# Optimization experiments

Hardware: AMD Instinct MI355X
Metric: run time of the kernel (lower is better)

The kernel has to match this reference:

```python
import jax, jax.numpy as jnp
import numpy as np

N_HEAD = 12

def _rotate_half(x):
    # interleaved rotation: (-x1, x0, -x3, x2, ...)
    x_even = x[..., ::2]
    x_odd = x[..., 1::2]
    return jnp.stack((-x_odd, x_even), axis=-1).reshape(x.shape)

def _rope_tables(T, D, dtype):
    inv_freq = 1.0 / (10000.0 ** (jnp.arange(0, D, 2, dtype=jnp.float32) / D))
    freqs = jnp.arange(T, dtype=jnp.float32)[:, None] * inv_freq[None, :]  # [T, D/2]
    cos = jnp.repeat(jnp.cos(freqs), 2, axis=-1).astype(dtype)  # [T, D]
    sin = jnp.repeat(jnp.sin(freqs), 2, axis=-1).astype(dtype)
    return cos, sin

def setup_inputs() -> dict:
    key = jax.random.key(0)
    ks = jax.random.split(key, 5)
    B, T, C = 8, 1024, 768
    return {
        "x": jax.random.normal(ks[0], (B, T, C), dtype=jnp.float32),
        "W_attn": jax.random.normal(ks[1], (C, 3 * C), dtype=jnp.float32) * (C ** -0.5),
        "b_attn": jax.random.normal(ks[2], (3 * C,), dtype=jnp.float32) * 0.02,
        "W_proj": jax.random.normal(ks[3], (C, C), dtype=jnp.float32) * (C ** -0.5),
        "b_proj": jax.random.normal(ks[4], (C,), dtype=jnp.float32) * 0.02,
    }

def reference(x, W_attn, b_attn, W_proj, b_proj):
    B, T, C = x.shape
    H = N_HEAD
    D = C // H
    qkv = x @ W_attn + b_attn  # [B, T, 3C]
    q, k, v = jnp.split(qkv, 3, axis=-1)
    # [B, H, T, D]
    q = q.reshape(B, T, H, D).transpose(0, 2, 1, 3)
    k = k.reshape(B, T, H, D).transpose(0, 2, 1, 3)
    v = v.reshape(B, T, H, D).transpose(0, 2, 1, 3)
    cos, sin = _rope_tables(T, D, x.dtype)  # [T, D]
    q = q * cos + _rotate_half(q) * sin
    k = k * cos + _rotate_half(k) * sin
    att = jnp.einsum('bhqd,bhkd->bhqk', q, k) * (D ** -0.5)
    causal = jnp.tril(jnp.ones((T, T), dtype=bool))
    att = jnp.where(causal, att, -jnp.inf)
    att = jax.nn.softmax(att, axis=-1)
    y = jnp.einsum('bhqk,bhkd->bhqd', att, v)  # [B, H, T, D]
    y = y.transpose(0, 2, 1, 3).reshape(B, T, C)
    return y @ W_proj + b_proj
```

## Files before the change

### kernel.cpp

```cpp
#include <hip/hip_runtime.h>
#include <cstdint>
#include <cstddef>

typedef __attribute__((ext_vector_type(8))) short frag8;
typedef __attribute__((ext_vector_type(4))) float facc4;

__device__ __forceinline__ float b2f(unsigned short u) {
  union { unsigned int i; float f; } v; v.i = ((unsigned int)u) << 16; return v.f;
}
__device__ __forceinline__ unsigned short f2b(float f) {
  union { float f; unsigned int i; } v; v.f = f;
  unsigned int u = v.i;
  unsigned int r = (u + 0x7fffu + ((u >> 16) & 1u)) >> 16;
  return (unsigned short)r;
}


__global__ void cvt_f32_bf16_k(const float* __restrict__ in, unsigned short* __restrict__ out, int n8) {
  int i = blockIdx.x * blockDim.x + threadIdx.x;
  if (i >= n8) return;
  const float4* p = (const float4*)in + (size_t)i * 2;
  float4 a = p[0], b = p[1];
  union { unsigned short u[8]; frag8 v; } o;
  o.u[0] = f2b(a.x); o.u[1] = f2b(a.y); o.u[2] = f2b(a.z); o.u[3] = f2b(a.w);
  o.u[4] = f2b(b.x); o.u[5] = f2b(b.y); o.u[6] = f2b(b.z); o.u[7] = f2b(b.w);
  *((frag8*)out + i) = o.v;
}

__global__ void transpose_cvt_k(const float* __restrict__ W, unsigned short* __restrict__ Wt, int R, int Cn) {
  __shared__ float tile[32][33];
  int tx = threadIdx.x, ty = threadIdx.y;
  int c = blockIdx.x * 32 + tx;
  #pragma unroll
  for (int i = 0; i < 32; i += 8)
    tile[ty + i][tx] = W[(size_t)(blockIdx.y * 32 + ty + i) * Cn + c];
  __syncthreads();
  int rr = blockIdx.y * 32 + tx;
  #pragma unroll
  for (int i = 0; i < 32; i += 8)
    Wt[(size_t)(blockIdx.x * 32 + ty + i) * R + rr] = f2b(tile[tx][ty + i]);
}

__global__ void rope_tables_k(float* __restrict__ cosT, float* __restrict__ sinT) {
  int id = blockIdx.x * 256 + threadIdx.x;
  int t = id >> 5, i = id & 31;
  float freq = powf(10000.0f, -(float)i * (1.0f / 32.0f));
  float a = (float)t * freq;
  cosT[id] = cosf(a);
  sinT[id] = sinf(a);
}

__global__ void rope_k(unsigned short* __restrict__ Q, unsigned short* __restrict__ Kb,
                       const float* __restrict__ cosT, const float* __restrict__ sinT) {
  int id = blockIdx.x * 256 + threadIdx.x;
  int i = id & 31;
  int t = (id >> 5) & 1023;
  int bh = id >> 15;
  size_t base = ((size_t)bh << 16) + (size_t)t * 64 + i * 2;
  float c = cosT[(t << 5) + i], s = sinT[(t << 5) + i];
  unsigned int* qp = (unsigned int*)(Q + base);
  unsigned int qu = *qp;
  float q0 = b2f(qu & 0xffffu), q1 = b2f(qu >> 16);
  *qp = (unsigned int)f2b(q0 * c - q1 * s) | ((unsigned int)f2b(q1 * c + q0 * s) << 16);
  unsigned int* kp = (unsigned int*)(Kb + base);
  unsigned int ku = *kp;
  float k0 = b2f(ku & 0xffffu), k1 = b2f(ku >> 16);
  *kp = (unsigned int)f2b(k0 * c - k1 * s) | ((unsigned int)f2b(k1 * c + k0 * s) << 16);
}


#define GLDK 72

template<int EPI>
__global__ __launch_bounds__(256)
void gemm128_k(const unsigned short* __restrict__ A, const unsigned short* __restrict__ Bt,
               const float* __restrict__ bias, float* __restrict__ outF,
               unsigned short* __restrict__ Qo, unsigned short* __restrict__ Ko,
               unsigned short* __restrict__ Vo, int M, int N, int K)
{
  __shared__ unsigned short As[128 * GLDK];
  __shared__ unsigned short Bs[128 * GLDK];
  const int tid = threadIdx.x;
  const int lane = tid & 63;
  const int w = tid >> 6, wm = w >> 1, wn = w & 1;
  const int g = lane >> 4, cL = lane & 15;
  const int tM = blockIdx.y * 128, tN = blockIdx.x * 128;

  facc4 zero4 = {0.f, 0.f, 0.f, 0.f};
  facc4 acc[4][4];
  #pragma unroll
  for (int i = 0; i < 4; ++i)
    #pragma unroll
    for (int j = 0; j < 4; ++j) acc[i][j] = zero4;

  const int sr = tid >> 3;
  const int sc = (tid & 7) * 8;

  for (int k0 = 0; k0 < K; k0 += 64) {
    #pragma unroll
    for (int ch = 0; ch < 4; ++ch) {
      int r = sr + ch * 32;
      frag8 va = *(const frag8*)(A  + (size_t)(tM + r) * K + k0 + sc);
      frag8 vb = *(const frag8*)(Bt + (size_t)(tN + r) * K + k0 + sc);
      *(frag8*)(&As[r * GLDK + sc]) = va;
      *(frag8*)(&Bs[r * GLDK + sc]) = vb;
    }
    __syncthreads();
    #pragma unroll
    for (int kk = 0; kk < 2; ++kk) {
      frag8 af[4], bfr[4];
      #pragma unroll
      for (int i = 0; i < 4; ++i)
        af[i] = *(const frag8*)(&As[(wm * 64 + i * 16 + cL) * GLDK + kk * 32 + g * 8]);
      #pragma unroll
      for (int j = 0; j < 4; ++j)
        bfr[j] = *(const frag8*)(&Bs[(wn * 64 + j * 16 + cL) * GLDK + kk * 32 + g * 8]);
      #pragma unroll
      for (int i = 0; i < 4; ++i)
        #pragma unroll
        for (int j = 0; j < 4; ++j)
          acc[i][j] = __builtin_amdgcn_mfma_f32_16x16x32_bf16(af[i], bfr[j], acc[i][j], 0, 0, 0);
    }
    __syncthreads();
  }

  #pragma unroll
  for (int i = 0; i < 4; ++i) {
    #pragma unroll
    for (int j = 0; j < 4; ++j) {
      const int col = tN + wn * 64 + j * 16 + cL;
      const float bv = bias[col];
      if constexpr (EPI == 0) {
        const int sel = col / 768;
        const int cc = col - sel * 768;
        const int h = cc >> 6, d = cc & 63;
        #pragma unroll
        for (int r = 0; r < 4; ++r) {
          const int m = tM + wm * 64 + i * 16 + g * 4 + r;
          const float v = acc[i][j][r] + bv;
          const int b = m >> 10, t = m & 1023;
          const size_t hb = ((size_t)(b * 12 + h)) << 16;
          if (sel == 0)      Qo[hb + (size_t)t * 64 + d] = f2b(v * 0.125f);
          else if (sel == 1) Ko[hb + (size_t)t * 64 + d] = f2b(v);
          else               Vo[hb + ((size_t)d << 10) + t] = f2b(v);
        }
      } else {
        #pragma unroll
        for (int r = 0; r < 4; ++r) {
          const int m = tM + wm * 64 + i * 16 + g * 4 + r;
          outF[(size_t)m * N + col] = acc[i][j][r] + bv;
        }
      }
    }
  }
}


__global__ __launch_bounds__(256, 4)
void attn_k(const unsigned short* __restrict__ Q, const unsigned short* __restrict__ Kb,
            const unsigned short* __restrict__ Vt, unsigned short* __restrict__ Y)
{
  __shared__ unsigned short Pl[4 * 16 * GLDK];
  const int tid = threadIdx.x, lane = tid & 63, w = tid >> 6;
  const int g = lane >> 4, cL = lane & 15;

  const int bid = blockIdx.x;
  const int xcd = bid & 7;
  const int slot = bid >> 3;
  const int bh = xcd + 8 * (slot % 12);
  const int qb = 15 - slot / 12;
  const int q0 = qb * 64;
  const int qw = q0 + w * 16;
  const size_t hb = ((size_t)bh) << 16;

  frag8 qf[2];
  #pragma unroll
  for (int ks = 0; ks < 2; ++ks)
    qf[ks] = *(const frag8*)(Q + hb + (size_t)(qw + cL) * 64 + ks * 32 + g * 8);

  const unsigned short* Kp = Kb + hb + (size_t)cL * 64 + g * 8;
  const unsigned short* Vp = Vt + hb + (size_t)cL * 1024;
  unsigned short* PlW = &Pl[w * (16 * GLDK)];

  facc4 zero4 = {0.f, 0.f, 0.f, 0.f};
  facc4 o[4];
  #pragma unroll
  for (int jd = 0; jd < 4; ++jd) o[jd] = zero4;
  float mrow[4] = {-1e30f, -1e30f, -1e30f, -1e30f};
  float lrow[4] = {0.f, 0.f, 0.f, 0.f};

  const int ntiles = qb + 1;
  for (int it = 0; it < ntiles; ++it) {
    const int kv0 = it * 64;
    facc4 s[4];
    #pragma unroll
    for (int j = 0; j < 4; ++j) s[j] = zero4;
    #pragma unroll
    for (int ks = 0; ks < 2; ++ks) {
      #pragma unroll
      for (int j = 0; j < 4; ++j) {
        frag8 kf = *(const frag8*)(Kp + (size_t)(kv0 + j * 16) * 64 + ks * 32);
        s[j] = __builtin_amdgcn_mfma_f32_16x16x32_bf16(qf[ks], kf, s[j], 0, 0, 0);
      }
    }
    frag8 vf[2][4];
    #pragma unroll
    for (int ks = 0; ks < 2; ++ks)
      #pragma unroll
      for (int jd = 0; jd < 4; ++jd)
        vf[ks][jd] = *(const frag8*)(Vp + (size_t)(jd * 16) * 1024 + kv0 + ks * 32 + g * 8);

    if (kv0 + 63 > qw) {
      #pragma unroll
      for (int j = 0; j < 4; ++j) {
        const int kcol = kv0 + j * 16 + cL;
        #pragma unroll
        for (int r = 0; r < 4; ++r)
          if (kcol > qw + g * 4 + r) s[j][r] = -1e30f;
      }
    }
    float pm[4];
    #pragma unroll
    for (int r = 0; r < 4; ++r)
      pm[r] = fmaxf(fmaxf(s[0][r], s[1][r]), fmaxf(s[2][r], s[3][r]));
    #pragma unroll
    for (int d = 8; d >= 1; d >>= 1)
      #pragma unroll
      for (int r = 0; r < 4; ++r)
        pm[r] = fmaxf(pm[r], __shfl_xor(pm[r], d));

    float sc_[4], rsum[4];
    #pragma unroll
    for (int r = 0; r < 4; ++r) {
      const float mn = fmaxf(mrow[r], pm[r]);
      sc_[r] = __expf(mrow[r] - mn);
      mrow[r] = mn;
      rsum[r] = 0.0f;
    }
    #pragma unroll
    for (int j = 0; j < 4; ++j)
      #pragma unroll
      for (int r = 0; r < 4; ++r) {
        const float p = __expf(s[j][r] - mrow[r]);
        s[j][r] = p;
        rsum[r] += p;
      }
    #pragma unroll
    for (int j = 0; j < 4; ++j)
      #pragma unroll
      for (int r = 0; r < 4; ++r)
        PlW[(g * 4 + r) * GLDK + j * 16 + cL] = f2b(s[j][r]);
    #pragma unroll
    for (int d = 8; d >= 1; d >>= 1)
      #pragma unroll
      for (int r = 0; r < 4; ++r)
        rsum[r] += __shfl_xor(rsum[r], d);
    #pragma unroll
    for (int r = 0; r < 4; ++r)
      lrow[r] = lrow[r] * sc_[r] + rsum[r];
    #pragma unroll
    for (int jd = 0; jd < 4; ++jd)
      #pragma unroll
      for (int r = 0; r < 4; ++r)
        o[jd][r] *= sc_[r];
    #pragma unroll
    for (int ks = 0; ks < 2; ++ks) {
      frag8 pa = *(const frag8*)(&PlW[cL * GLDK + ks * 32 + g * 8]);
      #pragma unroll
      for (int jd = 0; jd < 4; ++jd)
        o[jd] = __builtin_amdgcn_mfma_f32_16x16x32_bf16(pa, vf[ks][jd], o[jd], 0, 0, 0);
    }
  }

  const int b = bh / 12, h = bh - (bh / 12) * 12;
  #pragma unroll
  for (int r = 0; r < 4; ++r) {
    const float inv = 1.0f / lrow[r];
    const int qrow = qw + g * 4 + r;
    #pragma unroll
    for (int jd = 0; jd < 4; ++jd)
      Y[(size_t)(b * 1024 + qrow) * 768 + h * 64 + jd * 16 + cL] = f2b(o[jd][r] * inv);
  }
}


extern "C" void kernel_launch(void* const* d_in, const int* in_sizes, int n_in,
                              void* d_out, int out_size, void* d_ws, size_t ws_size,
                              hipStream_t stream) {
  const float* x      = (const float*)d_in[0];
  const float* W_attn = (const float*)d_in[1];
  const float* b_attn = (const float*)d_in[2];
  const float* W_proj = (const float*)d_in[3];
  const float* b_proj = (const float*)d_in[4];
  float* out = (float*)d_out;
  char* ws = (char*)d_ws;

  unsigned short* xb  = (unsigned short*)(ws);
  unsigned short* WtA = (unsigned short*)(ws + 12582912);
  unsigned short* WtP = (unsigned short*)(ws + 16121856);
  unsigned short* Qb  = (unsigned short*)(ws + 17301504);
  unsigned short* Kb  = (unsigned short*)(ws + 29884416);
  unsigned short* Vt  = (unsigned short*)(ws + 42467328);
  unsigned short* Yb  = (unsigned short*)(ws + 55050240);
  float* cosT = (float*)(ws + 67633152);
  float* sinT = (float*)(ws + 67764224);

  cvt_f32_bf16_k<<<3072, 256, 0, stream>>>(x, xb, 786432);
  transpose_cvt_k<<<dim3(72, 24), dim3(32, 8), 0, stream>>>(W_attn, WtA, 768, 2304);
  transpose_cvt_k<<<dim3(24, 24), dim3(32, 8), 0, stream>>>(W_proj, WtP, 768, 768);
  rope_tables_k<<<128, 256, 0, stream>>>(cosT, sinT);
  gemm128_k<0><<<dim3(18, 64), 256, 0, stream>>>(xb, WtA, b_attn, nullptr, Qb, Kb, Vt, 8192, 2304, 768);
  rope_k<<<12288, 256, 0, stream>>>(Qb, Kb, cosT, sinT);
  attn_k<<<1536, 256, 0, stream>>>(Qb, Kb, Vt, Yb);
  gemm128_k<1><<<dim3(6, 64), 256, 0, stream>>>(Yb, WtP, b_proj, out, nullptr, nullptr, nullptr, 8192, 768, 768);
}
```

Before: 290.5 us.

## Transpose attention MFMA operands so each lane owns a query row; swizzle GEMM tiles

The attention kernel swaps the MFMA operand order so S^T and O^T are computed, which places one query row per lane column. Row max and sum then need only two cross-lane shuffles instead of four per row, and P and Y can be written with packed 64-bit bf16 stores. K fragments are also loaded up front before the QK MFMAs. The GEMM kernel adds an XCD-aware block-index swizzle meant to improve L2 locality, which assumes the block count divides evenly by 8.

```diff
diff --git a/kernel.cpp b/kernel.cpp
--- a/kernel.cpp
+++ b/kernel.cpp
@@ -1,4 +1,5 @@
 #include <hip/hip_runtime.h>
+#include <hip/hip_bf16.h>
 #include <cstdint>
 #include <cstddef>
 
@@ -13,6 +14,12 @@
   unsigned int u = v.i;
   unsigned int r = (u + 0x7fffu + ((u >> 16) & 1u)) >> 16;
   return (unsigned short)r;
+}
+__device__ __forceinline__ unsigned long long pk4(float a, float b, float c, float d) {
+  union { __hip_bfloat162 h2[2]; unsigned long long u; } pk;
+  pk.h2[0] = __float22bfloat162_rn(float2{a, b});
+  pk.h2[1] = __float22bfloat162_rn(float2{c, d});
+  return pk.u;
 }
 
 
@@ -84,7 +91,12 @@
   const int lane = tid & 63;
   const int w = tid >> 6, wm = w >> 1, wn = w & 1;
   const int g = lane >> 4, cL = lane & 15;
-  const int tM = blockIdx.y * 128, tN = blockIdx.x * 128;
+
+  const int nwg = gridDim.x * gridDim.y;
+  const int flat = blockIdx.y * gridDim.x + blockIdx.x;
+  const int cpx = nwg >> 3;
+  const int swz = (flat & 7) * cpx + (flat >> 3);
+  const int tM = (swz / gridDim.x) * 128, tN = (swz % gridDim.x) * 128;
 
   facc4 zero4 = {0.f, 0.f, 0.f, 0.f};
   facc4 acc[4][4];
@@ -169,8 +181,7 @@
   const int slot = bid >> 3;
   const int bh = xcd + 8 * (slot % 12);
   const int qb = 15 - slot / 12;
-  const int q0 = qb * 64;
-  const int qw = q0 + w * 16;
+  const int qw = qb * 64 + w * 16;
   const size_t hb = ((size_t)bh) << 16;
 
   frag8 qf[2];
@@ -179,108 +190,94 @@
     qf[ks] = *(const frag8*)(Q + hb + (size_t)(qw + cL) * 64 + ks * 32 + g * 8);
 
   const unsigned short* Kp = Kb + hb + (size_t)cL * 64 + g * 8;
-  const unsigned short* Vp = Vt + hb + (size_t)cL * 1024;
+  const unsigned short* Vp = Vt + hb + (size_t)cL * 1024 + g * 8;
   unsigned short* PlW = &Pl[w * (16 * GLDK)];
 
   facc4 zero4 = {0.f, 0.f, 0.f, 0.f};
   facc4 o[4];
   #pragma unroll
   for (int jd = 0; jd < 4; ++jd) o[jd] = zero4;
-  float mrow[4] = {-1e30f, -1e30f, -1e30f, -1e30f};
-  float lrow[4] = {0.f, 0.f, 0.f, 0.f};
+  float mrow = -1e30f, lrow = 0.f;
 
   const int ntiles = qb + 1;
   for (int it = 0; it < ntiles; ++it) {
     const int kv0 = it * 64;
+    frag8 kf[2][4];
+    #pragma unroll
+    for (int ks = 0; ks < 2; ++ks)
+      #pragma unroll
+      for (int j = 0; j < 4; ++j)
+        kf[ks][j] = *(const frag8*)(Kp + (size_t)(kv0 + j * 16) * 64 + ks * 32);
     facc4 s[4];
     #pragma unroll
     for (int j = 0; j < 4; ++j) s[j] = zero4;
     #pragma unroll
-    for (int ks = 0; ks < 2; ++ks) {
-      #pragma unroll
-      for (int j = 0; j < 4; ++j) {
-        frag8 kf = *(const frag8*)(Kp + (size_t)(kv0 + j * 16) * 64 + ks * 32);
-        s[j] = __builtin_amdgcn_mfma_f32_16x16x32_bf16(qf[ks], kf, s[j], 0, 0, 0);
-      }
-    }
+    for (int ks = 0; ks < 2; ++ks)
+      #pragma unroll
+      for (int j = 0; j < 4; ++j)
+        s[j] = __builtin_amdgcn_mfma_f32_16x16x32_bf16(kf[ks][j], qf[ks], s[j], 0, 0, 0);
     frag8 vf[2][4];
     #pragma unroll
     for (int ks = 0; ks < 2; ++ks)
       #pragma unroll
       for (int jd = 0; jd < 4; ++jd)
-        vf[ks][jd] = *(const frag8*)(Vp + (size_t)(jd * 16) * 1024 + kv0 + ks * 32 + g * 8);
+        vf[ks][jd] = *(const frag8*)(Vp + (size_t)(jd * 16) * 1024 + kv0 + ks * 32);
 
     if (kv0 + 63 > qw) {
-      #pragma unroll
-      for (int j = 0; j < 4; ++j) {
-        const int kcol = kv0 + j * 16 + cL;
+      const int qrow = qw + cL;
+      #pragma unroll
+      for (int j = 0; j < 4; ++j)
         #pragma unroll
         for (int r = 0; r < 4; ++r)
-          if (kcol > qw + g * 4 + r) s[j][r] = -1e30f;
+          if (kv0 + j * 16 + g * 4 + r > qrow) s[j][r] = -1e30f;
+    }
+    float pm = fmaxf(fmaxf(fmaxf(s[0][0], s[0][1]), fmaxf(s[0][2], s[0][3])),
+                     fmaxf(fmaxf(s[1][0], s[1][1]), fmaxf(s[1][2], s[1][3])));
+    pm = fmaxf(pm, fmaxf(fmaxf(fmaxf(s[2][0], s[2][1]), fmaxf(s[2][2], s[2][3])),
+                         fmaxf(fmaxf(s[3][0], s[3][1]), fmaxf(s[3][2], s[3][3]))));
+    pm = fmaxf(pm, __shfl_xor(pm, 16));
+    pm = fmaxf(pm, __shfl_xor(pm, 32));
+
+    const float mn = fmaxf(mrow, pm);
+    const float sc_ = __expf(mrow - mn);
+    mrow = mn;
+    float rs = 0.f;
+    #pragma unroll
+    for (int j = 0; j < 4; ++j)
+      #pragma unroll
+      for (int r = 0; r < 4; ++r) {
+        const float p = __expf(s[j][r] - mn);
+        s[j][r] = p;
+        rs += p;
       }
-    }
-    float pm[4];
-    #pragma unroll
-    for (int r = 0; r < 4; ++r)
-      pm[r] = fmaxf(fmaxf(s[0][r], s[1][r]), fmaxf(s[2][r], s[3][r]));
-    #pragma unroll
-    for (int d = 8; d >= 1; d >>= 1)
+    #pragma unroll
+    for (int j = 0; j < 4; ++j)
+      *(unsigned long long*)(&PlW[cL * GLDK + j * 16 + g * 4]) =
+          pk4(s[j][0], s[j][1], s[j][2], s[j][3]);
+    rs += __shfl_xor(rs, 16);
+    rs += __shfl_xor(rs, 32);
+    lrow = lrow * sc_ + rs;
+    #pragma unroll
+    for (int jd = 0; jd < 4; ++jd)
       #pragma unroll
       for (int r = 0; r < 4; ++r)
-        pm[r] = fmaxf(pm[r], __shfl_xor(pm[r], d));
-
-    float sc_[4], rsum[4];
-    #pragma unroll
-    for (int r = 0; r < 4; ++r) {
-      const float mn = fmaxf(mrow[r], pm[r]);
-      sc_[r] = __expf(mrow[r] - mn);
-      mrow[r] = mn;
-      rsum[r] = 0.0f;
-    }
-    #pragma unroll
-    for (int j = 0; j < 4; ++j)
-      #pragma unroll
-      for (int r = 0; r < 4; ++r) {
-        const float p = __expf(s[j][r] - mrow[r]);
-        s[j][r] = p;
-        rsum[r] += p;
-      }
-    #pragma unroll
-    for (int j = 0; j < 4; ++j)
-      #pragma unroll
-      for (int r = 0; r < 4; ++r)
-        PlW[(g * 4 + r) * GLDK + j * 16 + cL] = f2b(s[j][r]);
-    #pragma unroll
-    for (int d = 8; d >= 1; d >>= 1)
-      #pragma unroll
-      for (int r = 0; r < 4; ++r)
-        rsum[r] += __shfl_xor(rsum[r], d);
-    #pragma unroll
-    for (int r = 0; r < 4; ++r)
-      lrow[r] = lrow[r] * sc_[r] + rsum[r];
-    #pragma unroll
-    for (int jd = 0; jd < 4; ++jd)
-      #pragma unroll
-      for (int r = 0; r < 4; ++r)
-        o[jd][r] *= sc_[r];
+        o[jd][r] *= sc_;
     #pragma unroll
     for (int ks = 0; ks < 2; ++ks) {
       frag8 pa = *(const frag8*)(&PlW[cL * GLDK + ks * 32 + g * 8]);
       #pragma unroll
       for (int jd = 0; jd < 4; ++jd)
-        o[jd] = __builtin_amdgcn_mfma_f32_16x16x32_bf16(pa, vf[ks][jd], o[jd], 0, 0, 0);
+        o[jd] = __builtin_amdgcn_mfma_f32_16x16x32_bf16(vf[ks][jd], pa, o[jd], 0, 0, 0);
     }
   }
 
   const int b = bh / 12, h = bh - (bh / 12) * 12;
-  #pragma unroll
-  for (int r = 0; r < 4; ++r) {
-    const float inv = 1.0f / lrow[r];
-    const int qrow = qw + g * 4 + r;
-    #pragma unroll
-    for (int jd = 0; jd < 4; ++jd)
-      Y[(size_t)(b * 1024 + qrow) * 768 + h * 64 + jd * 16 + cL] = f2b(o[jd][r] * inv);
-  }
+  const float inv = 1.0f / lrow;
+  const size_t yrow = (size_t)(b * 1024 + qw + cL) * 768 + h * 64;
+  #pragma unroll
+  for (int jd = 0; jd < 4; ++jd)
+    *(unsigned long long*)(&Y[yrow + jd * 16 + g * 4]) =
+        pk4(o[jd][0] * inv, o[jd][1] * inv, o[jd][2] * inv, o[jd][3] * inv);
 }
 
 
```

Result: no change. 291.0 us (+0.2%).
